# Kernel tuning notes

Hardware: AMD Instinct MI355X
Metric: run time of the kernel (lower is better)

The kernel has to match this reference:

```python
import jax, jax.numpy as jnp
import numpy as np

BATCH = 2048
NUM_CLASSES = 100000
FEAT_DIM = 128


def setup_inputs() -> dict:
    key = jax.random.key(0)
    k1, k2, k3 = jax.random.split(key, 3)
    x = jax.random.normal(k1, (BATCH, FEAT_DIM), dtype=jnp.float32)
    labels = jax.random.randint(k2, (BATCH,), 0, NUM_CLASSES, dtype=jnp.int64)
    centers = jax.random.normal(k3, (NUM_CLASSES, FEAT_DIM), dtype=jnp.float32)
    return {"x": x, "labels": labels, "centers": centers}


def reference(x, labels, centers):
    x = x.astype(jnp.float32)
    x_sq = jnp.sum(x * x, axis=1, keepdims=True)            # (B, 1)
    c_sq = jnp.sum(centers * centers, axis=1)[None, :]      # (1, C)
    distmat = x_sq + c_sq - 2.0 * jnp.einsum('bd,cd->bc', x, centers)  # (B, C)
    classes = jnp.arange(centers.shape[0])
    mask = (labels[:, None] == classes[None, :]).astype(jnp.float32)   # (B, C)
    dist = distmat * mask
    # torch clamps AFTER masking, so the (C-1) zeros per row become 1e-12 each
    loss = jnp.sum(jnp.clip(dist, 1e-12, 1e12)) / x.shape[0]
    return loss
```

## Files before the change

### kernel.cpp

```cpp
#include <hip/hip_runtime.h>


#define CL_BATCH 2048
#define CL_CLASSES 100000
#define CL_FEAT 128
#define CL_WAVES 4
#define CL_BLOCKS (CL_BATCH / CL_WAVES)

__global__ void __launch_bounds__(256)
cl_dist_kernel(const float* __restrict__ x,
               const int* __restrict__ labels,
               const float* __restrict__ centers,
               float* __restrict__ partial) {
    const int wave = threadIdx.x >> 6;
    const int lane = threadIdx.x & 63;
    const int b = blockIdx.x * CL_WAVES + wave;

    const float2* xp = reinterpret_cast<const float2*>(x + (size_t)b * CL_FEAT);
    const int lab = labels[b];
    const float2* cp = reinterpret_cast<const float2*>(centers + (size_t)lab * CL_FEAT);

    const float2 xv = xp[lane];
    const float2 cv = cp[lane];
    const float dx = xv.x - cv.x;
    const float dy = xv.y - cv.y;
    float s = dx * dx + dy * dy;

    #pragma unroll
    for (int off = 32; off > 0; off >>= 1)
        s += __shfl_down(s, off, 64);

    __shared__ float wsum[CL_WAVES];
    if (lane == 0) {
        s = fminf(fmaxf(s, 1e-12f), 1e12f);
        wsum[wave] = s;
    }
    __syncthreads();
    if (threadIdx.x == 0) {
        float t = 0.0f;
        #pragma unroll
        for (int i = 0; i < CL_WAVES; ++i) t += wsum[i];
        partial[blockIdx.x] = t;
    }
}

__global__ void __launch_bounds__(512)
cl_reduce_kernel(const float* __restrict__ partial, float* __restrict__ out) {
    const int tid = threadIdx.x;
    float s = partial[tid];

    #pragma unroll
    for (int off = 32; off > 0; off >>= 1)
        s += __shfl_down(s, off, 64);

    __shared__ float wsum[8];
    const int wave = tid >> 6;
    const int lane = tid & 63;
    if (lane == 0) wsum[wave] = s;
    __syncthreads();
    if (tid == 0) {
        float t = 0.0f;
        #pragma unroll
        for (int i = 0; i < 8; ++i) t += wsum[i];
        const float clamp_const = (float)(CL_CLASSES - 1) * 1e-12f;
        out[0] = t / (float)CL_BATCH + clamp_const;
    }
}

extern "C" void kernel_launch(void* const* d_in, const int* in_sizes, int n_in,
                              void* d_out, int out_size, void* d_ws, size_t ws_size,
                              hipStream_t stream) {
    const float* x       = (const float*)d_in[0];
    const int*   labels  = (const int*)d_in[1];
    const float* centers = (const float*)d_in[2];
    float* out = (float*)d_out;
    float* partial = (float*)d_ws;

    cl_dist_kernel<<<CL_BLOCKS, 256, 0, stream>>>(x, labels, centers, partial);
    cl_reduce_kernel<<<1, 512, 0, stream>>>(partial, out);
}
```

Baseline: 11.76 us.

## Fuse distance and reduction kernels via cooperative launch with grid sync

Merges the per-row distance kernel and the final reduction into one cooperatively launched kernel: 64 blocks of 1024 threads, with each wave handling two rows, followed by a grid-wide sync and a single-wave final reduction. The aim is to remove the second kernel launch and its launch gap. In exchange it adds the cost of a grid barrier and a cooperative launch path, which can carry its own overhead.

```diff
diff --git a/kernel.cpp b/kernel.cpp
--- a/kernel.cpp
+++ b/kernel.cpp
@@ -1,69 +1,65 @@
 #include <hip/hip_runtime.h>
+#include <hip/hip_cooperative_groups.h>
+
+namespace cg = cooperative_groups;
 
 
 #define CL_BATCH 2048
 #define CL_CLASSES 100000
 #define CL_FEAT 128
-#define CL_WAVES 4
-#define CL_BLOCKS (CL_BATCH / CL_WAVES)
+#define CL_BLOCKS 64
+#define CL_THREADS 1024
+#define CL_WPB (CL_THREADS / 64)
+#define CL_RPW (CL_BATCH / (CL_BLOCKS * CL_WPB))
 
-__global__ void __launch_bounds__(256)
-cl_dist_kernel(const float* __restrict__ x,
-               const int* __restrict__ labels,
-               const float* __restrict__ centers,
-               float* __restrict__ partial) {
-    const int wave = threadIdx.x >> 6;
+__global__ void __launch_bounds__(CL_THREADS)
+cl_fused_kernel(const float* __restrict__ x,
+                const int* __restrict__ labels,
+                const float* __restrict__ centers,
+                float* __restrict__ partial,
+                float* __restrict__ out) {
+    const int wid  = threadIdx.x >> 6;
     const int lane = threadIdx.x & 63;
-    const int b = blockIdx.x * CL_WAVES + wave;
+    const int gw   = blockIdx.x * CL_WPB + wid;
 
-    const float2* xp = reinterpret_cast<const float2*>(x + (size_t)b * CL_FEAT);
-    const int lab = labels[b];
-    const float2* cp = reinterpret_cast<const float2*>(centers + (size_t)lab * CL_FEAT);
+    float wsum = 0.0f;
+    #pragma unroll
+    for (int r = 0; r < CL_RPW; ++r) {
+        const int b = gw * CL_RPW + r;
+        const float2 xv =
+            reinterpret_cast<const float2*>(x + (size_t)b * CL_FEAT)[lane];
+        const int lab = labels[b];
+        const float2 cv =
+            reinterpret_cast<const float2*>(centers + (size_t)lab * CL_FEAT)[lane];
+        const float dx = xv.x - cv.x;
+        const float dy = xv.y - cv.y;
+        float s = dx * dx + dy * dy;
+        #pragma unroll
+        for (int off = 32; off > 0; off >>= 1)
+            s += __shfl_down(s, off, 64);
+        if (lane == 0)
+            wsum += fminf(fmaxf(s, 1e-12f), 1e12f);
+    }
 
-    const float2 xv = xp[lane];
-    const float2 cv = cp[lane];
-    const float dx = xv.x - cv.x;
-    const float dy = xv.y - cv.y;
-    float s = dx * dx + dy * dy;
-
-    #pragma unroll
-    for (int off = 32; off > 0; off >>= 1)
-        s += __shfl_down(s, off, 64);
-
-    __shared__ float wsum[CL_WAVES];
-    if (lane == 0) {
-        s = fminf(fmaxf(s, 1e-12f), 1e12f);
-        wsum[wave] = s;
-    }
+    __shared__ float smem[CL_WPB];
+    if (lane == 0) smem[wid] = wsum;
     __syncthreads();
     if (threadIdx.x == 0) {
         float t = 0.0f;
         #pragma unroll
-        for (int i = 0; i < CL_WAVES; ++i) t += wsum[i];
+        for (int i = 0; i < CL_WPB; ++i) t += smem[i];
         partial[blockIdx.x] = t;
     }
-}
 
-__global__ void __launch_bounds__(512)
-cl_reduce_kernel(const float* __restrict__ partial, float* __restrict__ out) {
-    const int tid = threadIdx.x;
-    float s = partial[tid];
+    cg::this_grid().sync();
 
-    #pragma unroll
-    for (int off = 32; off > 0; off >>= 1)
-        s += __shfl_down(s, off, 64);
-
-    __shared__ float wsum[8];
-    const int wave = tid >> 6;
-    const int lane = tid & 63;
-    if (lane == 0) wsum[wave] = s;
-    __syncthreads();
-    if (tid == 0) {
-        float t = 0.0f;
+    if (blockIdx.x == 0 && threadIdx.x < 64) {
+        float s = partial[lane];
         #pragma unroll
-        for (int i = 0; i < 8; ++i) t += wsum[i];
-        const float clamp_const = (float)(CL_CLASSES - 1) * 1e-12f;
-        out[0] = t / (float)CL_BATCH + clamp_const;
+        for (int off = 32; off > 0; off >>= 1)
+            s += __shfl_down(s, off, 64);
+        if (lane == 0)
+            out[0] = s / (float)CL_BATCH + (float)(CL_CLASSES - 1) * 1e-12f;
     }
 }
 
@@ -73,9 +69,12 @@
     const float* x       = (const float*)d_in[0];
     const int*   labels  = (const int*)d_in[1];
     const float* centers = (const float*)d_in[2];
-    float* out = (float*)d_out;
+    float* out     = (float*)d_out;
     float* partial = (float*)d_ws;
 
-    cl_dist_kernel<<<CL_BLOCKS, 256, 0, stream>>>(x, labels, centers, partial);
-    cl_reduce_kernel<<<1, 512, 0, stream>>>(partial, out);
+    void* args[] = {(void*)&x, (void*)&labels, (void*)&centers,
+                    (void*)&partial, (void*)&out};
+    hipLaunchCooperativeKernel(reinterpret_cast<void*>(cl_fused_kernel),
+                               dim3(CL_BLOCKS), dim3(CL_THREADS),
+                               args, 0, stream);
 }
```

Result: slower. 32.59 us (+177.2%).
